# Kernel optimization log

Hardware: AMD Instinct MI355X
Metric: run time of the kernel (lower is better)

Reference implementation:

```python
import jax, jax.numpy as jnp
import numpy as np

T, D_ENC, H, D_EMB, VOCAB = 4000, 1024, 1024, 512, 8192
V = VOCAB + 1  # + blank
P = 800
TEMPERATURE = 1.0


def setup_inputs() -> dict:
    key = jax.random.key(0)
    ks = jax.random.split(key, 8)
    s = lambda d: 1.0 / np.sqrt(d)
    return {
        'enc_out': jax.random.normal(ks[0], (T, D_ENC), jnp.float32),
        'embedding': jax.random.normal(ks[1], (V, D_EMB), jnp.float32) * s(D_EMB),
        'W_ih': jax.random.normal(ks[2], (4 * H, D_EMB), jnp.float32) * s(D_EMB),
        'W_hh': jax.random.normal(ks[3], (4 * H, H), jnp.float32) * s(H),
        'b_lstm': jnp.zeros((4 * H,), jnp.float32),
        'W_pred': jax.random.normal(ks[4], (D_ENC, H), jnp.float32) * s(H),
        'b_pred': jnp.zeros((D_ENC,), jnp.float32),
        'W_join': jax.random.normal(ks[5], (V, D_ENC), jnp.float32) * s(D_ENC),
        'b_join': jnp.zeros((V,), jnp.float32),
        'phonemes': jax.random.randint(ks[6], (P,), 0, VOCAB, jnp.int32),
    }


def reference(enc_out, embedding, W_ih, W_hh, b_lstm, W_pred, b_pred, W_join, b_join, phonemes):
    blank_idx = embedding.shape[0] - 1
    n_phon = phonemes.shape[0]

    def predict_step(tok, h, c):
        # one-token RNNT predictor: embed -> LSTM cell -> projection to joiner dim
        x = embedding[tok]
        gates = x @ W_ih.T + h @ W_hh.T + b_lstm  # [4H]
        i, f, g, o = jnp.split(gates, 4)
        i, f, o = jax.nn.sigmoid(i), jax.nn.sigmoid(f), jax.nn.sigmoid(o)
        c2 = f * c + i * jnp.tanh(g)
        h2 = o * jnp.tanh(c2)
        pred = h2 @ W_pred.T + b_pred  # [D_ENC]
        return pred, h2, c2

    def step(carry, enc_t):
        tok, h, c, tp = carry
        pred, h2, c2 = predict_step(tok, h, c)
        logits = (jax.nn.relu(enc_t + pred) @ W_join.T + b_join) / TEMPERATURE
        logp = jax.nn.log_softmax(logits)  # [V]
        pick = jnp.argmax(logp)
        phon_done = tp >= n_phon
        is_blank = (pick == blank_idx) | phon_done
        next_phon = phonemes[jnp.minimum(tp, n_phon - 1)]
        prediction = jnp.where(is_blank, blank_idx, next_phon)
        # blank: keep hypothesis token/state; non-blank: advance to phoneme + new state
        tok2 = jnp.where(is_blank, tok, next_phon)
        h3 = jnp.where(is_blank, h, h2)
        c3 = jnp.where(is_blank, c, c2)
        tp2 = tp + jnp.where(is_blank, 0, 1)
        return (tok2, h3, c3, tp2), (logp, prediction, ~phon_done)

    # initial predictor pass with blank token from zero state (mirrors the warm-up predict call)
    h0 = jnp.zeros((W_hh.shape[1],), enc_out.dtype)
    c0 = jnp.zeros_like(h0)
    _, h_init, c_init = predict_step(jnp.int32(blank_idx), h0, c0)
    carry0 = (jnp.int32(blank_idx), h_init, c_init, jnp.int32(0))
    _, (alignment, predictions, valid) = jax.lax.scan(step, carry0, enc_out)
    return alignment, predictions, valid
```

## Files before the change

kernel.cpp:

```cpp
#include <hip/hip_runtime.h>
#include <math.h>

#define TT     4000
#define DENC   1024
#define HD     1024
#define DEMB   512
#define VD     8193
#define NPH    800
#define BLANK  8192
#define NWG    256
#define NTHR   512
#define CHUNK  256
#define CHUNK_M 800
#define NSTEP  (NPH + 2)
#define NVT    65
#define NP     129

typedef __bf16 bf16x4 __attribute__((ext_vector_type(4)));
typedef __bf16 bf16x8 __attribute__((ext_vector_type(8)));
typedef float  f32x16 __attribute__((ext_vector_type(16)));

#define FLAGS_BYTES  4096
#define MEMSET_BYTES 20480
#define WSF_HX     1024
#define WSF_HHIST  5120
#define WSF_PREDS  826368
#define WSF_PMAX_M 1646592
#define WSF_PSUM_M 2162592
#define WSF_PARG_M 2678592
#define WSF_LSE_M  3194592
#define WSF_AMAX_M 3198592
#define WSF_W16    3199616
#define WSF_XBF    7459456
#define WSF_END_M  9163392
#define NEED_MFMA  ((size_t)WSF_END_M * 4)
#define F_PMAX 1646592
#define F_PSUM 1906592
#define F_PARG 2166592
#define F_LSE  2426592

#define S_XH   0
#define S_GS   3072
#define S_C4   3088
#define S_TOK  3264
#define S_RED  4066
#define S_AMAX 4082
#define SMEM_FLOATS_F32 4352
#define SMEM_BYTES_F32 (SMEM_FLOATS_F32 * 4)
#define SMEM_BYTES_MFMA (65536 + 128)

struct Ctx {
  const float *enc, *emb, *Wih, *Whh, *bl, *Wpred, *bp, *Wjoin, *bj;
  const int* phon;
  unsigned long long* hx;
  float *hhist, *preds, *pmax, *psum, *lse;
  int* parg;
  int* amaxws;
  __bf16 *w16, *xbf;
  unsigned* flags;
  float *out_align, *out_pred, *out_valid;
};

__device__ __forceinline__ float dot4(float4 a, float4 b, float acc) {
  acc = fmaf(a.x, b.x, acc); acc = fmaf(a.y, b.y, acc);
  acc = fmaf(a.z, b.z, acc); acc = fmaf(a.w, b.w, acc);
  return acc;
}
__device__ __forceinline__ float sigmf(float x) { return 1.f / (1.f + expf(-x)); }

__device__ __forceinline__ void combine3(float& m, float& s, int& am,
                                         float om, float os, int oa) {
  float mm = fmaxf(m, om);
  s = s * __expf(m - mm) + os * __expf(om - mm);
  if (om > m || (om == m && oa < am)) am = oa;
  m = mm;
}

__device__ __forceinline__ void gload16(const void* g, void* l) {
  __builtin_amdgcn_global_load_lds(
      (const __attribute__((address_space(1))) unsigned int*)g,
      (__attribute__((address_space(3))) unsigned int*)l, 16, 0, 0);
}

__device__ __forceinline__ void light_barrier(unsigned* flags, unsigned& ep) {
  unsigned* arrive  = flags;
  unsigned* release = flags + 256;
  __builtin_amdgcn_s_waitcnt(0);
  __syncthreads();
  if (blockIdx.x == 0) {
    int tid = threadIdx.x;
    if (tid > 0 && tid < NWG) {
      while (__hip_atomic_load(&arrive[tid], __ATOMIC_RELAXED, __HIP_MEMORY_SCOPE_AGENT) != ep) {}
    }
    __syncthreads();
    if (tid == 0)
      __hip_atomic_store(release, ep, __ATOMIC_RELAXED, __HIP_MEMORY_SCOPE_AGENT);
  } else {
    if (threadIdx.x == 0) {
      __hip_atomic_store(&arrive[blockIdx.x], ep, __ATOMIC_RELAXED, __HIP_MEMORY_SCOPE_AGENT);
      while (__hip_atomic_load(release, __ATOMIC_RELAXED, __HIP_MEMORY_SCOPE_AGENT) != ep) {}
    }
    __syncthreads();
  }
  asm volatile("" ::: "memory");
  ep++;
}

__device__ __forceinline__ void heavy_barrier(unsigned* flags) {
  unsigned* bar = flags + 257;
  __syncthreads();
  if (threadIdx.x == 0) {
    __threadfence();
    unsigned g = __hip_atomic_load(&bar[1], __ATOMIC_RELAXED, __HIP_MEMORY_SCOPE_AGENT);
    unsigned v = __hip_atomic_fetch_add(&bar[0], 1u, __ATOMIC_RELAXED, __HIP_MEMORY_SCOPE_AGENT);
    if (v == (unsigned)(NWG - 1)) {
      __hip_atomic_store(&bar[0], 0u, __ATOMIC_RELAXED, __HIP_MEMORY_SCOPE_AGENT);
      __hip_atomic_store(&bar[1], g + 1u, __ATOMIC_RELEASE, __HIP_MEMORY_SCOPE_AGENT);
    } else {
      while (__hip_atomic_load(&bar[1], __ATOMIC_RELAXED, __HIP_MEMORY_SCOPE_AGENT) == g)
        __builtin_amdgcn_s_sleep(1);
    }
    __threadfence();
  }
  __syncthreads();
}

__device__ __forceinline__ float ld_coh(const float* p) {
  return __hip_atomic_load((const float*)p, __ATOMIC_RELAXED, __HIP_MEMORY_SCOPE_AGENT);
}

__device__ void chain_all(const Ctx& C, float* sm) {
  const int tid = threadIdx.x;
  const int w = tid >> 6, l = tid & 63;
  const int b = blockIdx.x;
  int* tok_sm = (int*)(sm + S_TOK);

  for (int s = tid; s < NSTEP; s += NTHR)
    tok_sm[s] = (s < 2) ? BLANK : C.phon[s - 2];

  float4 W0[6], W1[6];
  {
    int rr0 = 2 * w, rr1 = 2 * w + 1;
    int gr0 = ((rr0 >> 2) << 10) + 4 * b + (rr0 & 3);
    int gr1 = ((rr1 >> 2) << 10) + 4 * b + (rr1 & 3);
    const float4* ih0 = (const float4*)(C.Wih + (size_t)gr0 * DEMB);
    const float4* hh0 = (const float4*)(C.Whh + (size_t)gr0 * HD);
    const float4* ih1 = (const float4*)(C.Wih + (size_t)gr1 * DEMB);
    const float4* hh1 = (const float4*)(C.Whh + (size_t)gr1 * HD);
    W0[0] = ih0[l];       W0[1] = ih0[64 + l];
    W0[2] = hh0[l];       W0[3] = hh0[64 + l];
    W0[4] = hh0[128 + l]; W0[5] = hh0[192 + l];
    W1[0] = ih1[l];       W1[1] = ih1[64 + l];
    W1[2] = hh1[l];       W1[3] = hh1[64 + l];
    W1[4] = hh1[128 + l]; W1[5] = hh1[192 + l];
  }
  float bi = 0.f, bf = 0.f, bg = 0.f, bo = 0.f;
  if (tid < 4) {
    bi = C.bl[4 * b + tid];
    bf = C.bl[1024 + 4 * b + tid];
    bg = C.bl[2048 + 4 * b + tid];
    bo = C.bl[3072 + 4 * b + tid];
    sm[S_C4 + tid] = 0.f;
  }
  for (int i = tid; i < 1536; i += NTHR) sm[S_XH + i] = 0.f;
  if (tid < 512) sm[S_XH + tid] = C.emb[(size_t)BLANK * DEMB + tid];
  __syncthreads();

  unsigned long long* hx = C.hx;
  for (int s = 0; s < NSTEP; ++s) {
    int p = s & 1;
    const float4* xh4 = (const float4*)(sm + S_XH + p * 1536);
    float a0 = 0.f, a1 = 0.f;
    #pragma unroll
    for (int i = 0; i < 6; ++i) {
      float4 v = xh4[i * 64 + l];
      a0 = dot4(W0[i], v, a0);
      a1 = dot4(W1[i], v, a1);
    }
    #pragma unroll
    for (int m = 32; m; m >>= 1) {
      a0 += __shfl_xor(a0, m, 64);
      a1 += __shfl_xor(a1, m, 64);
    }
    if (l == 0) { sm[S_GS + 2 * w] = a0; sm[S_GS + 2 * w + 1] = a1; }
    if (s + 1 < NSTEP && tid < 512)
      sm[S_XH + (1 - p) * 1536 + tid] = C.emb[(size_t)tok_sm[s + 1] * DEMB + tid];
    __syncthreads();
    if (tid < 4) {
      int j = tid;
      float gi = sm[S_GS + j]      + bi;
      float gf = sm[S_GS + 4 + j]  + bf;
      float gg = sm[S_GS + 8 + j]  + bg;
      float go = sm[S_GS + 12 + j] + bo;
      float cc = sm[S_C4 + j];
      float c2 = sigmf(gf) * cc + sigmf(gi) * tanhf(gg);
      float h2 = sigmf(go) * tanhf(c2);
      sm[S_C4 + j] = c2;
      int cell = 4 * b + j;
      C.hhist[(size_t)s * HD + cell] = h2;
      unsigned long long pk = ((unsigned long long)(unsigned)(s + 1) << 32)
                            | (unsigned long long)__float_as_uint(h2);
      __hip_atomic_store(&hx[(1 - p) * 1024 + cell], pk,
                         __ATOMIC_RELAXED, __HIP_MEMORY_SCOPE_AGENT);
    }
    if (s + 1 < NSTEP) {
      unsigned tg = (unsigned)(s + 1);
      #pragma unroll
      for (int kq = 0; kq < 2; ++kq) {
        int k = tid + kq * 512;
        unsigned long long v;
        do {
          v = __hip_atomic_load(&hx[(1 - p) * 1024 + k],
                                __ATOMIC_RELAXED, __HIP_MEMORY_SCOPE_AGENT);
        } while ((unsigned)(v >> 32) != tg);
        sm[S_XH + (1 - p) * 1536 + 512 + k] = __uint_as_float((unsigned)v);
      }
    }
    __syncthreads();
  }
}

__device__ void preds_gemm(const Ctx& C, float* sm) {
  float* Wt = sm;
  float* Xt = sm + 2112;
  const int tid = threadIdx.x;
  const int tx = tid & 31, ty = tid >> 5;
  const int NJT = (NPH + 1 + 63) >> 6;
  int ntiles = 8 * NJT;
  for (int tile = blockIdx.x; tile < ntiles; tile += NWG) {
    int vt = tile & 7, jt = tile >> 3;
    int v0 = vt * 128, j0 = jt * 64;
    float acc[4][4];
    #pragma unroll
    for (int a = 0; a < 4; ++a)
      #pragma unroll
      for (int q = 0; q < 4; ++q) acc[a][q] = 0.f;
    for (int kk = 0; kk < 1024; kk += 16) {
      {
        int r = tid >> 2, seg = tid & 3;
        float4 wv = ((const float4*)(C.Wpred + (size_t)(v0 + r) * HD + kk))[seg];
        Wt[(seg * 4 + 0) * 132 + r] = wv.x;
        Wt[(seg * 4 + 1) * 132 + r] = wv.y;
        Wt[(seg * 4 + 2) * 132 + r] = wv.z;
        Wt[(seg * 4 + 3) * 132 + r] = wv.w;
      }
      if (tid < 256) {
        int r = tid >> 2, seg = tid & 3;
        int j = j0 + r;
        float4 xv = make_float4(0.f, 0.f, 0.f, 0.f);
        if (j <= NPH) xv = ((const float4*)(C.hhist + (size_t)(j + 1) * HD + kk))[seg];
        Xt[(seg * 4 + 0) * 68 + r] = xv.x;
        Xt[(seg * 4 + 1) * 68 + r] = xv.y;
        Xt[(seg * 4 + 2) * 68 + r] = xv.z;
        Xt[(seg * 4 + 3) * 68 + r] = xv.w;
      }
      __syncthreads();
      #pragma unroll
      for (int k = 0; k < 16; ++k) {
        float4 a = *(const float4*)(Wt + k * 132 + (tx << 2));
        float4 bq = *(const float4*)(Xt + k * 68 + (ty << 2));
        acc[0][0] = fmaf(a.x, bq.x, acc[0][0]); acc[1][0] = fmaf(a.y, bq.x, acc[1][0]);
        acc[2][0] = fmaf(a.z, bq.x, acc[2][0]); acc[3][0] = fmaf(a.w, bq.x, acc[3][0]);
        acc[0][1] = fmaf(a.x, bq.y, acc[0][1]); acc[1][1] = fmaf(a.y, bq.y, acc[1][1]);
        acc[2][1] = fmaf(a.z, bq.y, acc[2][1]); acc[3][1] = fmaf(a.w, bq.y, acc[3][1]);
        acc[0][2] = fmaf(a.x, bq.z, acc[0][2]); acc[1][2] = fmaf(a.y, bq.z, acc[1][2]);
        acc[2][2] = fmaf(a.z, bq.z, acc[2][2]); acc[3][2] = fmaf(a.w, bq.z, acc[3][2]);
        acc[0][3] = fmaf(a.x, bq.w, acc[0][3]); acc[1][3] = fmaf(a.y, bq.w, acc[1][3]);
        acc[2][3] = fmaf(a.z, bq.w, acc[2][3]); acc[3][3] = fmaf(a.w, bq.w, acc[3][3]);
      }
      __syncthreads();
    }
    int vb = v0 + (tx << 2), jb0 = j0 + (ty << 2);
    #pragma unroll
    for (int jj = 0; jj < 4; ++jj) {
      int j = jb0 + jj;
      if (j > NPH) continue;
      #pragma unroll
      for (int q = 0; q < 4; ++q)
        C.preds[(size_t)j * 1024 + vb + q] = acc[q][jj] + C.bp[vb + q];
    }
  }
}


__device__ void xbf_pass(const Ctx& C, int t0, int K, int pi0) {
  int g0 = blockIdx.x * NTHR + threadIdx.x;
  int total = K << 8;
  for (int q = g0; q < total; q += NWG * NTHR) {
    int j = q >> 8, seg = q & 255;
    int pi = (pi0 < 0) ? NPH : pi0 + j;
    float4 e = ((const float4*)(C.enc + (size_t)(t0 + j) * 1024))[seg];
    float4 p = ((const float4*)(C.preds + (size_t)pi * 1024))[seg];
    bf16x4 r;
    r[0] = (__bf16)fmaxf(e.x + p.x, 0.f);
    r[1] = (__bf16)fmaxf(e.y + p.y, 0.f);
    r[2] = (__bf16)fmaxf(e.z + p.z, 0.f);
    r[3] = (__bf16)fmaxf(e.w + p.w, 0.f);
    *(bf16x4*)(C.xbf + (size_t)j * 1024 + (seg << 2)) = r;
  }
}

__device__ void joiner_mfma(const Ctx& C, char* smc, int t0, int K) {
  const int tid = threadIdx.x;
  const int wid = tid >> 6, lane = tid & 63;
  const int wj = wid & 3, wv = wid >> 2;
  const int l31 = lane & 31, lhi = lane >> 5;
  const int jt_n = (K + 127) >> 7;
  const int ntiles = jt_n * NVT;
  const __bf16* W16 = C.w16;
  const __bf16* Xbf = C.xbf;

  for (int tile = blockIdx.x; tile < ntiles; tile += NWG) {
    const int vt = tile % NVT, jt = tile / NVT;
    const int v0 = vt << 7, j0 = jt << 7;
    f32x16 acc0, acc1;
    #pragma unroll
    for (int i = 0; i < 16; ++i) { acc0[i] = 0.f; acc1[i] = 0.f; }

    auto stage = [&](int db, int kb) {
      char* wb = smc + db * 32768;
      char* xb = wb + 16384;
      #pragma unroll
      for (int p = 0; p < 2; ++p) {
        int sbase = p * 512 + wid * 64;
        int s = sbase + lane;
        int ks = s >> 7, r = s & 127;
        gload16(W16 + (size_t)(v0 + r) * 1024 + kb + ks * 8, wb + sbase * 16);
        gload16(Xbf + (size_t)(j0 + r) * 1024 + kb + ks * 8, xb + sbase * 16);
      }
    };

    stage(0, 0);
    __syncthreads();
    int db = 0;
    for (int kb16 = 0; kb16 < 16; ++kb16) {
      if (kb16 < 15) stage(db ^ 1, (kb16 + 1) << 6);
      const char* wb = smc + db * 32768;
      const char* xb = wb + 16384;
      #pragma unroll
      for (int k16 = 0; k16 < 4; ++k16) {
        int ks = k16 * 2 + lhi;
        bf16x8 a  = *(const bf16x8*)(xb + ((ks << 7) + (wj << 5) + l31) * 16);
        bf16x8 b0 = *(const bf16x8*)(wb + ((ks << 7) + (wv << 6) + l31) * 16);
        bf16x8 b1 = *(const bf16x8*)(wb + ((ks << 7) + (wv << 6) + 32 + l31) * 16);
        acc0 = __builtin_amdgcn_mfma_f32_32x32x16_bf16(a, b0, acc0, 0, 0, 0);
        acc1 = __builtin_amdgcn_mfma_f32_32x32x16_bf16(a, b1, acc1, 0, 0, 0);
      }
      __syncthreads();
      db ^= 1;
    }

    const int v_0 = v0 + (wv << 6) + l31;
    const int v_1 = v_0 + 32;
    const float bj0 = (v_0 < VD) ? C.bj[v_0] : 0.f;
    const float bj1 = (v_1 < VD) ? C.bj[v_1] : 0.f;
    const int jbase = j0 + (wj << 5) + 4 * lhi;
    const bool npok = (v0 + (wv << 6)) < VD;
    const int np = (v0 >> 6) + wv;
    #pragma unroll
    for (int reg = 0; reg < 16; ++reg) {
      int j = jbase + (reg & 3) + 8 * (reg >> 2);
      bool jok = j < K;
      float lg0 = acc0[reg] + bj0;
      float lg1 = acc1[reg] + bj1;
      if (jok) {
        size_t ro = (size_t)(t0 + j) * VD;
        if (v_0 < VD) C.out_align[ro + v_0] = lg0;
        if (v_1 < VD) C.out_align[ro + v_1] = lg1;
      }
      float l0 = (v_0 < VD) ? lg0 : -1e30f;
      float l1 = (v_1 < VD) ? lg1 : -1e30f;
      float m = fmaxf(l0, l1);
      float ss = 0.f;
      if (v_0 < VD) ss += __expf(l0 - m);
      if (v_1 < VD) ss += __expf(l1 - m);
      int am = (l1 > l0) ? v_1 : v_0;
      #pragma unroll
      for (int msk = 1; msk <= 16; msk <<= 1) {
        float om = __shfl_xor(m, msk, 64);
        float os = __shfl_xor(ss, msk, 64);
        int oa = __shfl_xor(am, msk, 64);
        float mm = fmaxf(m, om);
        ss = ss * __expf(m - mm) + os * __expf(om - mm);
        if (om > m || (om == m && oa < am)) am = oa;
        m = mm;
      }
      if (l31 == 0 && jok && npok) {
        size_t pb = (size_t)(t0 + j) * NP + np;
        __hip_atomic_store(&C.pmax[pb], m, __ATOMIC_RELAXED, __HIP_MEMORY_SCOPE_AGENT);
        __hip_atomic_store(&C.psum[pb], ss, __ATOMIC_RELAXED, __HIP_MEMORY_SCOPE_AGENT);
        __hip_atomic_store(&C.parg[pb], am, __ATOMIC_RELAXED, __HIP_MEMORY_SCOPE_AGENT);
      }
    }
  }
}

__device__ __forceinline__ void merge_row129(const Ctx& C, int row, int lane,
                                             float& m, float& s, int& am) {
  size_t b = (size_t)row * NP;
  m = ld_coh(C.pmax + b + lane);
  s = ld_coh(C.psum + b + lane);
  am = __hip_atomic_load(&C.parg[b + lane], __ATOMIC_RELAXED, __HIP_MEMORY_SCOPE_AGENT);
  {
    int i2 = lane + 64;
    float om = ld_coh(C.pmax + b + i2);
    float os = ld_coh(C.psum + b + i2);
    int oa = __hip_atomic_load(&C.parg[b + i2], __ATOMIC_RELAXED, __HIP_MEMORY_SCOPE_AGENT);
    combine3(m, s, am, om, os, oa);
  }
  if (lane == 0) {
    float om = ld_coh(C.pmax + b + 128);
    float os = ld_coh(C.psum + b + 128);
    int oa = __hip_atomic_load(&C.parg[b + 128], __ATOMIC_RELAXED, __HIP_MEMORY_SCOPE_AGENT);
    combine3(m, s, am, om, os, oa);
  }
  #pragma unroll
  for (int msk = 32; msk; msk >>= 1) {
    float om = __shfl_xor(m, msk, 64);
    float os = __shfl_xor(s, msk, 64);
    int oa = __shfl_xor(am, msk, 64);
    combine3(m, s, am, om, os, oa);
  }
}

__global__ __launch_bounds__(NTHR) void decode_kernel_mfma(
    const float* enc, const float* emb, const float* Wih, const float* Whh,
    const float* bl, const float* Wpred, const float* bp, const float* Wjoin,
    const float* bj, const int* phon, float* out, float* wsf) {
  extern __shared__ float sm[];
  char* smc = (char*)sm;
  Ctx C;
  C.enc = enc; C.emb = emb; C.Wih = Wih; C.Whh = Whh; C.bl = bl;
  C.Wpred = Wpred; C.bp = bp; C.Wjoin = Wjoin; C.bj = bj; C.phon = phon;
  C.flags = (unsigned*)wsf;
  C.hx = (unsigned long long*)(wsf + WSF_HX);
  C.hhist = wsf + WSF_HHIST;
  C.preds = wsf + WSF_PREDS;
  C.pmax = wsf + WSF_PMAX_M;
  C.psum = wsf + WSF_PSUM_M;
  C.parg = (int*)(wsf + WSF_PARG_M);
  C.lse = wsf + WSF_LSE_M;
  C.amaxws = (int*)(wsf + WSF_AMAX_M);
  C.w16 = (__bf16*)(wsf + WSF_W16);
  C.xbf = (__bf16*)(wsf + WSF_XBF);
  C.out_align = out;
  C.out_pred  = out + (size_t)TT * VD;
  C.out_valid = out + (size_t)TT * VD + TT;

  const int tid = threadIdx.x;
  const int wid = tid >> 6, lane = tid & 63;
  unsigned ep = 1;

  {
    int g0 = blockIdx.x * NTHR + tid;
    for (int q = g0; q < VD * 256; q += NWG * NTHR) {
      int v = q >> 8, seg = q & 255;
      float4 w4 = ((const float4*)(C.Wjoin + (size_t)v * 1024))[seg];
      bf16x4 r;
      r[0] = (__bf16)w4.x; r[1] = (__bf16)w4.y; r[2] = (__bf16)w4.z; r[3] = (__bf16)w4.w;
      *(bf16x4*)(C.w16 + (size_t)v * 1024 + (seg << 2)) = r;
    }
  }

  chain_all(C, sm);
  heavy_barrier(C.flags);
  preds_gemm(C, sm);
  heavy_barrier(C.flags);

  int t = 0, tp = 0;
  while (t < TT && tp < NPH) {
    int K = CHUNK_M;
    if (TT - t < K) K = TT - t;
    if (NPH - tp < K) K = NPH - tp;
    heavy_barrier(C.flags);
    xbf_pass(C, t, K, tp);
    heavy_barrier(C.flags);
    joiner_mfma(C, smc, t, K);
    light_barrier(C.flags, ep);

    for (int j = blockIdx.x * 8 + wid; j < K; j += NWG * 8) {
      float m, s; int am;
      merge_row129(C, t + j, lane, m, s, am);
      if (lane == 0) {
        __hip_atomic_store(&C.amaxws[j], am, __ATOMIC_RELAXED, __HIP_MEMORY_SCOPE_AGENT);
        C.lse[t + j] = m + logf(s);
      }
    }
    light_barrier(C.flags, ep);

    int cand = K;
    for (int idx = tid; idx < K; idx += NTHR) {
      int a = __hip_atomic_load(&C.amaxws[idx], __ATOMIC_RELAXED, __HIP_MEMORY_SCOPE_AGENT);
      if (a == BLANK && idx < cand) cand = idx;
    }
    #pragma unroll
    for (int msk = 32; msk; msk >>= 1) cand = min(cand, __shfl_xor(cand, msk, 64));
    int* red = (int*)(smc + 65536);
    if (lane == 0) red[wid] = cand;
    __syncthreads();
    if (tid == 0) {
      int mn = red[0];
      for (int w2 = 1; w2 < 8; ++w2) mn = min(mn, red[w2]);
      red[8] = mn;
    }
    __syncthreads();
    int jb = red[8];
    __syncthreads();
    int nacc = (jb < K) ? jb + 1 : K;
    int nadv = (jb < K) ? jb : K;
    if (blockIdx.x == 0) {
      for (int j = tid; j < nacc; j += NTHR) {
        C.out_pred[t + j] = (j == jb) ? (float)BLANK : (float)C.phon[tp + j];
        C.out_valid[t + j] = 1.f;
      }
    }
    t += nacc; tp += nadv;
  }

  if (t < TT) {
    int Kt = TT - t;
    heavy_barrier(C.flags);
    xbf_pass(C, t, Kt, -1);
    heavy_barrier(C.flags);
    joiner_mfma(C, smc, t, Kt);
    light_barrier(C.flags, ep);
    for (int j = blockIdx.x * 8 + wid; j < Kt; j += NWG * 8) {
      float m, s; int am;
      merge_row129(C, t + j, lane, m, s, am);
      if (lane == 0) C.lse[t + j] = m + logf(s);
    }
    const int gtid = blockIdx.x * NTHR + tid;
    for (int i = gtid; i < Kt; i += NWG * NTHR) {
      C.out_pred[t + i] = (float)BLANK;
      C.out_valid[t + i] = 0.f;
    }
  }

  heavy_barrier(C.flags);

  for (int row = blockIdx.x; row < TT; row += NWG) {
    float l = C.lse[row];
    float* p = C.out_align + (size_t)row * VD;
    for (int i = tid; i < VD; i += NTHR) p[i] -= l;
  }
}


__device__ void joiner_gemm_f32(const Ctx& C, float* sm, int t0, int K, int pi0) {
  float* Wt = sm;
  float* Xt = sm + 2112;
  const int tid = threadIdx.x;
  const int tx = tid & 31, ty = tid >> 5;
  int jt_n = (K + 63) >> 6;
  int ntiles = jt_n * NVT;
  for (int tile = blockIdx.x; tile < ntiles; tile += NWG) {
    int vt = tile % NVT, jt = tile / NVT;
    int v0 = vt * 128, j0 = jt * 64;
    float acc[4][4];
    #pragma unroll
    for (int a = 0; a < 4; ++a)
      #pragma unroll
      for (int q = 0; q < 4; ++q) acc[a][q] = 0.f;

    for (int kk = 0; kk < 1024; kk += 16) {
      {
        int r = tid >> 2, seg = tid & 3;
        int v = v0 + r;
        float4 wv = make_float4(0.f, 0.f, 0.f, 0.f);
        if (v < VD) wv = ((const float4*)(C.Wjoin + (size_t)v * 1024 + kk))[seg];
        Wt[(seg * 4 + 0) * 132 + r] = wv.x;
        Wt[(seg * 4 + 1) * 132 + r] = wv.y;
        Wt[(seg * 4 + 2) * 132 + r] = wv.z;
        Wt[(seg * 4 + 3) * 132 + r] = wv.w;
      }
      if (tid < 256) {
        int r = tid >> 2, seg = tid & 3;
        int j = j0 + r;
        float4 xv = make_float4(0.f, 0.f, 0.f, 0.f);
        if (j < K) {
          int pi = (pi0 < 0) ? NPH : (pi0 + j);
          float4 e = ((const float4*)(C.enc + (size_t)(t0 + j) * DENC + kk))[seg];
          float4 pr = ((const float4*)(C.preds + (size_t)pi * 1024 + kk))[seg];
          xv.x = fmaxf(e.x + pr.x, 0.f);
          xv.y = fmaxf(e.y + pr.y, 0.f);
          xv.z = fmaxf(e.z + pr.z, 0.f);
          xv.w = fmaxf(e.w + pr.w, 0.f);
        }
        Xt[(seg * 4 + 0) * 68 + r] = xv.x;
        Xt[(seg * 4 + 1) * 68 + r] = xv.y;
        Xt[(seg * 4 + 2) * 68 + r] = xv.z;
        Xt[(seg * 4 + 3) * 68 + r] = xv.w;
      }
      __syncthreads();
      #pragma unroll
      for (int k = 0; k < 16; ++k) {
        float4 a = *(const float4*)(Wt + k * 132 + (tx << 2));
        float4 bq = *(const float4*)(Xt + k * 68 + (ty << 2));
        acc[0][0] = fmaf(a.x, bq.x, acc[0][0]); acc[1][0] = fmaf(a.y, bq.x, acc[1][0]);
        acc[2][0] = fmaf(a.z, bq.x, acc[2][0]); acc[3][0] = fmaf(a.w, bq.x, acc[3][0]);
        acc[0][1] = fmaf(a.x, bq.y, acc[0][1]); acc[1][1] = fmaf(a.y, bq.y, acc[1][1]);
        acc[2][1] = fmaf(a.z, bq.y, acc[2][1]); acc[3][1] = fmaf(a.w, bq.y, acc[3][1]);
        acc[0][2] = fmaf(a.x, bq.z, acc[0][2]); acc[1][2] = fmaf(a.y, bq.z, acc[1][2]);
        acc[2][2] = fmaf(a.z, bq.z, acc[2][2]); acc[3][2] = fmaf(a.w, bq.z, acc[3][2]);
        acc[0][3] = fmaf(a.x, bq.w, acc[0][3]); acc[1][3] = fmaf(a.y, bq.w, acc[1][3]);
        acc[2][3] = fmaf(a.z, bq.w, acc[2][3]); acc[3][3] = fmaf(a.w, bq.w, acc[3][3]);
      }
      __syncthreads();
    }
    int vb = v0 + (tx << 2);
    int jb0 = j0 + (ty << 2);
    float bjv[4];
    #pragma unroll
    for (int q = 0; q < 4; ++q) bjv[q] = (vb + q < VD) ? C.bj[vb + q] : 0.f;
    #pragma unroll
    for (int jj = 0; jj < 4; ++jj) {
      int j = jb0 + jj;
      if (j >= K) continue;
      size_t ro = (size_t)(t0 + j) * VD;
      float lg[4];
      float m = -1e30f; int am = vb;
      #pragma unroll
      for (int q = 0; q < 4; ++q) {
        int v = vb + q;
        if (v < VD) {
          lg[q] = acc[q][jj] + bjv[q];
          C.out_align[ro + v] = lg[q];
          if (lg[q] > m) { m = lg[q]; am = v; }
        } else lg[q] = -1e30f;
      }
      float ss = 0.f;
      #pragma unroll
      for (int q = 0; q < 4; ++q)
        if (vb + q < VD) ss += __expf(lg[q] - m);
      #pragma unroll
      for (int msk = 16; msk; msk >>= 1) {
        float om = __shfl_xor(m, msk, 64);
        float os = __shfl_xor(ss, msk, 64);
        int oa = __shfl_xor(am, msk, 64);
        combine3(m, ss, am, om, os, oa);
      }
      if (tx == 0) {
        size_t pb = (size_t)(t0 + j) * NVT + vt;
        __hip_atomic_store(&C.pmax[pb], m, __ATOMIC_RELAXED, __HIP_MEMORY_SCOPE_AGENT);
        __hip_atomic_store(&C.psum[pb], ss, __ATOMIC_RELAXED, __HIP_MEMORY_SCOPE_AGENT);
        __hip_atomic_store(&C.parg[pb], am, __ATOMIC_RELAXED, __HIP_MEMORY_SCOPE_AGENT);
      }
    }
  }
}

__device__ __forceinline__ void merge_row65(const Ctx& C, int row, int lane,
                                            float& m, float& s, int& am) {
  size_t b = (size_t)row * NVT;
  m = ld_coh(C.pmax + b + lane);
  s = ld_coh(C.psum + b + lane);
  am = __hip_atomic_load(&C.parg[b + lane], __ATOMIC_RELAXED, __HIP_MEMORY_SCOPE_AGENT);
  if (lane == 0) {
    float om = ld_coh(C.pmax + b + 64);
    float os = ld_coh(C.psum + b + 64);
    int oa = __hip_atomic_load(&C.parg[b + 64], __ATOMIC_RELAXED, __HIP_MEMORY_SCOPE_AGENT);
    combine3(m, s, am, om, os, oa);
  }
  #pragma unroll
  for (int msk = 32; msk; msk >>= 1) {
    float om = __shfl_xor(m, msk, 64);
    float os = __shfl_xor(s, msk, 64);
    int oa = __shfl_xor(am, msk, 64);
    combine3(m, s, am, om, os, oa);
  }
}

__global__ __launch_bounds__(NTHR) void decode_kernel_f32(
    const float* enc, const float* emb, const float* Wih, const float* Whh,
    const float* bl, const float* Wpred, const float* bp, const float* Wjoin,
    const float* bj, const int* phon, float* out, float* wsf) {
  extern __shared__ float sm[];
  Ctx C;
  C.enc = enc; C.emb = emb; C.Wih = Wih; C.Whh = Whh; C.bl = bl;
  C.Wpred = Wpred; C.bp = bp; C.Wjoin = Wjoin; C.bj = bj; C.phon = phon;
  C.flags = (unsigned*)wsf;
  C.hx = (unsigned long long*)(wsf + WSF_HX);
  C.hhist = wsf + WSF_HHIST;
  C.preds = wsf + WSF_PREDS;
  C.pmax = wsf + F_PMAX;
  C.psum = wsf + F_PSUM;
  C.parg = (int*)(wsf + F_PARG);
  C.lse = wsf + F_LSE;
  C.amaxws = 0; C.w16 = 0; C.xbf = 0;
  C.out_align = out;
  C.out_pred  = out + (size_t)TT * VD;
  C.out_valid = out + (size_t)TT * VD + TT;

  const int tid = threadIdx.x;
  const int wid = tid >> 6, lane = tid & 63;
  unsigned ep = 1;

  chain_all(C, sm);
  heavy_barrier(C.flags);
  preds_gemm(C, sm);
  heavy_barrier(C.flags);

  int t = 0, tp = 0;
  while (t < TT && tp < NPH) {
    int K = CHUNK;
    if (TT - t < K) K = TT - t;
    if (NPH - tp < K) K = NPH - tp;
    joiner_gemm_f32(C, sm, t, K, tp);
    light_barrier(C.flags, ep);

    int* amax_l = (int*)(sm + S_AMAX);
    for (int j = wid; j < K; j += 8) {
      float m, s; int am;
      merge_row65(C, t + j, lane, m, s, am);
      if (lane == 0) {
        amax_l[j] = am;
        C.lse[t + j] = m + logf(s);
      }
    }
    __syncthreads();
    int cand = K;
    if (tid < K && amax_l[tid] == BLANK) cand = tid;
    #pragma unroll
    for (int msk = 32; msk; msk >>= 1) cand = min(cand, __shfl_xor(cand, msk, 64));
    int* red = (int*)(sm + S_RED);
    if (lane == 0) red[wid] = cand;
    __syncthreads();
    if (tid == 0) {
      int mn = red[0];
      for (int w2 = 1; w2 < 8; ++w2) mn = min(mn, red[w2]);
      red[8] = mn;
    }
    __syncthreads();
    int jb = red[8];
    __syncthreads();
    int nacc = (jb < K) ? jb + 1 : K;
    int nadv = (jb < K) ? jb : K;
    if (blockIdx.x == 0) {
      int* tok_sm = (int*)(sm + S_TOK);
      for (int j = tid; j < nacc; j += NTHR) {
        C.out_pred[t + j] = (j == jb) ? (float)BLANK : (float)tok_sm[tp + j + 2];
        C.out_valid[t + j] = 1.f;
      }
    }
    t += nacc; tp += nadv;
    if (jb < K) heavy_barrier(C.flags);
  }

  if (t < TT) {
    int Kt = TT - t;
    joiner_gemm_f32(C, sm, t, Kt, -1);
    light_barrier(C.flags, ep);
    for (int i = blockIdx.x * 8 + wid; i < Kt; i += NWG * 8) {
      float m, s; int am;
      merge_row65(C, t + i, lane, m, s, am);
      if (lane == 0) C.lse[t + i] = m + logf(s);
    }
    const int gtid = blockIdx.x * NTHR + tid;
    for (int i = gtid; i < Kt; i += NWG * NTHR) {
      C.out_pred[t + i] = (float)BLANK;
      C.out_valid[t + i] = 0.f;
    }
  }

  heavy_barrier(C.flags);

  for (int row = blockIdx.x; row < TT; row += NWG) {
    float l = C.lse[row];
    float* p = C.out_align + (size_t)row * VD;
    for (int i = tid; i < VD; i += NTHR) p[i] -= l;
  }
}

extern "C" void kernel_launch(void* const* d_in, const int* in_sizes, int n_in,
                              void* d_out, int out_size, void* d_ws, size_t ws_size,
                              hipStream_t stream) {
  const float* enc   = (const float*)d_in[0];
  const float* emb   = (const float*)d_in[1];
  const float* Wih   = (const float*)d_in[2];
  const float* Whh   = (const float*)d_in[3];
  const float* bl    = (const float*)d_in[4];
  const float* Wpred = (const float*)d_in[5];
  const float* bp    = (const float*)d_in[6];
  const float* Wjoin = (const float*)d_in[7];
  const float* bj    = (const float*)d_in[8];
  const int*   phon  = (const int*)d_in[9];
  float* out = (float*)d_out;
  float* wsf = (float*)d_ws;

  hipMemsetAsync(d_ws, 0, MEMSET_BYTES, stream);

  void* args[] = { &enc, &emb, &Wih, &Whh, &bl, &Wpred, &bp, &Wjoin, &bj, &phon, &out, &wsf };
  if (ws_size >= NEED_MFMA) {
    hipFuncSetAttribute((const void*)decode_kernel_mfma,
                        hipFuncAttributeMaxDynamicSharedMemorySize, SMEM_BYTES_MFMA);
    hipError_t e = hipLaunchCooperativeKernel((void*)decode_kernel_mfma, dim3(NWG), dim3(NTHR),
                                              args, SMEM_BYTES_MFMA, stream);
    if (e != hipSuccess) {
      decode_kernel_mfma<<<dim3(NWG), dim3(NTHR), SMEM_BYTES_MFMA, stream>>>(
          enc, emb, Wih, Whh, bl, Wpred, bp, Wjoin, bj, phon, out, wsf);
    }
  } else {
    hipFuncSetAttribute((const void*)decode_kernel_f32,
                        hipFuncAttributeMaxDynamicSharedMemorySize, SMEM_BYTES_F32);
    hipError_t e = hipLaunchCooperativeKernel((void*)decode_kernel_f32, dim3(NWG), dim3(NTHR),
                                              args, SMEM_BYTES_F32, stream);
    if (e != hipSuccess) {
      decode_kernel_f32<<<dim3(NWG), dim3(NTHR), SMEM_BYTES_F32, stream>>>(
          enc, emb, Wih, Whh, bl, Wpred, bp, Wjoin, bj, phon, out, wsf);
    }
  }
}
```

Before: 2.850 ms.

## Split monolithic cooperative decode into staged kernels with speculative joiner

Replaces the single cooperative MFMA decode kernel with a pipeline of separate kernels: Wjoin bf16 conversion, a batched input-gate GEMM over all phoneme embeddings, a recurrence-only LSTM chain kernel holding W_hh in registers, a predictor GEMM, a speculative joiner over precomputed rows, a cooperative decode kernel, a tail joiner and final log-softmax subtraction. It moves the embedding-to-gate work off the serial recurrence and uses fast exp-based sigmoid/tanh. The aim is to shorten the sequential critical path and avoid grid-wide barriers between phases. The cost is more kernel launches and possibly wasted speculative joiner work, plus slightly lower-precision activations.

```diff
diff --git a/kernel.cpp b/kernel.cpp
--- a/kernel.cpp
+++ b/kernel.cpp
@@ -10,35 +10,40 @@
 #define BLANK  8192
 #define NWG    256
 #define NTHR   512
-#define CHUNK  256
 #define CHUNK_M 800
 #define NSTEP  (NPH + 2)
+#define NSTEPP 802
 #define NVT    65
 #define NP     129
+#define CHUNK  256
 
 typedef __bf16 bf16x4 __attribute__((ext_vector_type(4)));
 typedef __bf16 bf16x8 __attribute__((ext_vector_type(8)));
 typedef float  f32x16 __attribute__((ext_vector_type(16)));
 
-#define FLAGS_BYTES  4096
 #define MEMSET_BYTES 20480
 #define WSF_HX     1024
 #define WSF_HHIST  5120
 #define WSF_PREDS  826368
-#define WSF_PMAX_M 1646592
-#define WSF_PSUM_M 2162592
-#define WSF_PARG_M 2678592
-#define WSF_LSE_M  3194592
-#define WSF_AMAX_M 3198592
-#define WSF_W16    3199616
-#define WSF_XBF    7459456
-#define WSF_END_M  9163392
-#define NEED_MFMA  ((size_t)WSF_END_M * 4)
+#define WSF_GXT    826368
+#define WSF_PMAX   1646592
+#define WSF_PSUM   2162592
+#define WSF_PARG   2678592
+#define WSF_LSE    3194592
+#define WSF_AMAX   3198592
+#define WSF_XBF    3199616
+#define WSF_W16    4903552
+#define WSF_END    9163392
+#define NEED_MFMA  ((size_t)WSF_END * 4)
+#define TST_IDX    512
 #define F_PMAX 1646592
 #define F_PSUM 1906592
 #define F_PARG 2166592
 #define F_LSE  2426592
 
+#define GEMM_SMEM  12800
+#define CHAIN_SMEM ((16 * NSTEPP + 2048 + 64) * 4)
+#define JOIN_SMEM  (65536 + 128)
 #define S_XH   0
 #define S_GS   3072
 #define S_C4   3088
@@ -47,19 +52,7 @@
 #define S_AMAX 4082
 #define SMEM_FLOATS_F32 4352
 #define SMEM_BYTES_F32 (SMEM_FLOATS_F32 * 4)
-#define SMEM_BYTES_MFMA (65536 + 128)
-
-struct Ctx {
-  const float *enc, *emb, *Wih, *Whh, *bl, *Wpred, *bp, *Wjoin, *bj;
-  const int* phon;
-  unsigned long long* hx;
-  float *hhist, *preds, *pmax, *psum, *lse;
-  int* parg;
-  int* amaxws;
-  __bf16 *w16, *xbf;
-  unsigned* flags;
-  float *out_align, *out_pred, *out_valid;
-};
+
 
 __device__ __forceinline__ float dot4(float4 a, float4 b, float acc) {
   acc = fmaf(a.x, b.x, acc); acc = fmaf(a.y, b.y, acc);
@@ -67,6 +60,11 @@
   return acc;
 }
 __device__ __forceinline__ float sigmf(float x) { return 1.f / (1.f + expf(-x)); }
+__device__ __forceinline__ float sigm_fast(float x) { return 1.f / (1.f + __expf(-x)); }
+__device__ __forceinline__ float tanh_fast(float x) {
+  float e = __expf(2.f * x);
+  return 1.f - 2.f / (e + 1.f);
+}
 
 __device__ __forceinline__ void combine3(float& m, float& s, int& am,
                                          float om, float os, int oa) {
@@ -80,6 +78,10 @@
   __builtin_amdgcn_global_load_lds(
       (const __attribute__((address_space(1))) unsigned int*)g,
       (__attribute__((address_space(3))) unsigned int*)l, 16, 0, 0);
+}
+
+__device__ __forceinline__ float ld_coh(const float* p) {
+  return __hip_atomic_load((const float*)p, __ATOMIC_RELAXED, __HIP_MEMORY_SCOPE_AGENT);
 }
 
 __device__ __forceinline__ void light_barrier(unsigned* flags, unsigned& ep) {
@@ -125,19 +127,521 @@
   __syncthreads();
 }
 
-__device__ __forceinline__ float ld_coh(const float* p) {
-  return __hip_atomic_load((const float*)p, __ATOMIC_RELAXED, __HIP_MEMORY_SCOPE_AGENT);
-}
-
-__device__ void chain_all(const Ctx& C, float* sm) {
+__device__ void xbf_fill(const float* enc, const float* preds, __bf16* dst,
+                         int t0, int K, int pi0, int g0, int gs) {
+  int total = K << 8;
+  for (int q = g0; q < total; q += gs) {
+    int j = q >> 8, seg = q & 255;
+    int pi = (pi0 < 0) ? NPH : pi0 + j;
+    float4 e = ((const float4*)(enc + (size_t)(t0 + j) * 1024))[seg];
+    float4 p = ((const float4*)(preds + (size_t)pi * 1024))[seg];
+    bf16x4 r;
+    r[0] = (__bf16)fmaxf(e.x + p.x, 0.f);
+    r[1] = (__bf16)fmaxf(e.y + p.y, 0.f);
+    r[2] = (__bf16)fmaxf(e.z + p.z, 0.f);
+    r[3] = (__bf16)fmaxf(e.w + p.w, 0.f);
+    *(bf16x4*)(dst + (size_t)j * 1024 + (seg << 2)) = r;
+  }
+}
+
+__device__ void joiner_tiles(const __bf16* W16, const __bf16* xrows, const float* bj,
+                             float* out_align, float* pmax, float* psum, int* parg,
+                             char* smc, int t0, int K, int tile0, int tstride) {
+  const int tid = threadIdx.x;
+  const int wid = tid >> 6, lane = tid & 63;
+  const int wj = wid & 3, wv = wid >> 2;
+  const int l31 = lane & 31, lhi = lane >> 5;
+  const int jt_n = (K + 127) >> 7;
+  const int ntiles = jt_n * NVT;
+
+  for (int tile = tile0; tile < ntiles; tile += tstride) {
+    const int vt = tile % NVT, jt = tile / NVT;
+    const int v0 = vt << 7, j0 = jt << 7;
+    f32x16 acc0, acc1;
+    #pragma unroll
+    for (int i = 0; i < 16; ++i) { acc0[i] = 0.f; acc1[i] = 0.f; }
+
+    auto stage = [&](int db, int kb) {
+      char* wb = smc + db * 32768;
+      char* xb = wb + 16384;
+      #pragma unroll
+      for (int p = 0; p < 2; ++p) {
+        int sbase = p * 512 + wid * 64;
+        int s = sbase + lane;
+        int ks = s >> 7, r = s & 127;
+        gload16(W16 + (size_t)(v0 + r) * 1024 + kb + ks * 8, wb + sbase * 16);
+        gload16(xrows + (size_t)(j0 + r) * 1024 + kb + ks * 8, xb + sbase * 16);
+      }
+    };
+
+    stage(0, 0);
+    __syncthreads();
+    int db = 0;
+    for (int kb16 = 0; kb16 < 16; ++kb16) {
+      if (kb16 < 15) stage(db ^ 1, (kb16 + 1) << 6);
+      const char* wb = smc + db * 32768;
+      const char* xb = wb + 16384;
+      #pragma unroll
+      for (int k16 = 0; k16 < 4; ++k16) {
+        int ks = k16 * 2 + lhi;
+        bf16x8 a  = *(const bf16x8*)(xb + ((ks << 7) + (wj << 5) + l31) * 16);
+        bf16x8 b0 = *(const bf16x8*)(wb + ((ks << 7) + (wv << 6) + l31) * 16);
+        bf16x8 b1 = *(const bf16x8*)(wb + ((ks << 7) + (wv << 6) + 32 + l31) * 16);
+        acc0 = __builtin_amdgcn_mfma_f32_32x32x16_bf16(a, b0, acc0, 0, 0, 0);
+        acc1 = __builtin_amdgcn_mfma_f32_32x32x16_bf16(a, b1, acc1, 0, 0, 0);
+      }
+      __syncthreads();
+      db ^= 1;
+    }
+
+    const int v_0 = v0 + (wv << 6) + l31;
+    const int v_1 = v_0 + 32;
+    const float bj0 = (v_0 < VD) ? bj[v_0] : 0.f;
+    const float bj1 = (v_1 < VD) ? bj[v_1] : 0.f;
+    const int jbase = j0 + (wj << 5) + 4 * lhi;
+    const bool npok = (v0 + (wv << 6)) < VD;
+    const int np = (v0 >> 6) + wv;
+    #pragma unroll
+    for (int reg = 0; reg < 16; ++reg) {
+      int j = jbase + (reg & 3) + 8 * (reg >> 2);
+      bool jok = j < K;
+      float lg0 = acc0[reg] + bj0;
+      float lg1 = acc1[reg] + bj1;
+      if (jok) {
+        size_t ro = (size_t)(t0 + j) * VD;
+        if (v_0 < VD) out_align[ro + v_0] = lg0;
+        if (v_1 < VD) out_align[ro + v_1] = lg1;
+      }
+      float l0 = (v_0 < VD) ? lg0 : -1e30f;
+      float l1 = (v_1 < VD) ? lg1 : -1e30f;
+      float m = fmaxf(l0, l1);
+      float ss = 0.f;
+      if (v_0 < VD) ss += __expf(l0 - m);
+      if (v_1 < VD) ss += __expf(l1 - m);
+      int am = (l1 > l0) ? v_1 : v_0;
+      #pragma unroll
+      for (int msk = 1; msk <= 16; msk <<= 1) {
+        float om = __shfl_xor(m, msk, 64);
+        float os = __shfl_xor(ss, msk, 64);
+        int oa = __shfl_xor(am, msk, 64);
+        float mm = fmaxf(m, om);
+        ss = ss * __expf(m - mm) + os * __expf(om - mm);
+        if (om > m || (om == m && oa < am)) am = oa;
+        m = mm;
+      }
+      if (l31 == 0 && jok && npok) {
+        size_t pb = (size_t)(t0 + j) * NP + np;
+        __hip_atomic_store(&pmax[pb], m, __ATOMIC_RELAXED, __HIP_MEMORY_SCOPE_AGENT);
+        __hip_atomic_store(&psum[pb], ss, __ATOMIC_RELAXED, __HIP_MEMORY_SCOPE_AGENT);
+        __hip_atomic_store(&parg[pb], am, __ATOMIC_RELAXED, __HIP_MEMORY_SCOPE_AGENT);
+      }
+    }
+  }
+}
+
+__device__ __forceinline__ void merge_row129(const float* pmax, const float* psum,
+                                             const int* parg, int row, int lane,
+                                             float& m, float& s, int& am) {
+  size_t b = (size_t)row * NP;
+  m = ld_coh(pmax + b + lane);
+  s = ld_coh(psum + b + lane);
+  am = __hip_atomic_load(&parg[b + lane], __ATOMIC_RELAXED, __HIP_MEMORY_SCOPE_AGENT);
+  {
+    int i2 = lane + 64;
+    float om = ld_coh(pmax + b + i2);
+    float os = ld_coh(psum + b + i2);
+    int oa = __hip_atomic_load(&parg[b + i2], __ATOMIC_RELAXED, __HIP_MEMORY_SCOPE_AGENT);
+    combine3(m, s, am, om, os, oa);
+  }
+  if (lane == 0) {
+    float om = ld_coh(pmax + b + 128);
+    float os = ld_coh(psum + b + 128);
+    int oa = __hip_atomic_load(&parg[b + 128], __ATOMIC_RELAXED, __HIP_MEMORY_SCOPE_AGENT);
+    combine3(m, s, am, om, os, oa);
+  }
+  #pragma unroll
+  for (int msk = 32; msk; msk >>= 1) {
+    float om = __shfl_xor(m, msk, 64);
+    float os = __shfl_xor(s, msk, 64);
+    int oa = __shfl_xor(am, msk, 64);
+    combine3(m, s, am, om, os, oa);
+  }
+}
+
+__global__ __launch_bounds__(512) void wconv_kernel(const float* __restrict__ Wjoin,
+                                                    float* wsf) {
+  __bf16* w16 = (__bf16*)(wsf + WSF_W16);
+  int g0 = blockIdx.x * 512 + threadIdx.x;
+  int gs = gridDim.x * 512;
+  for (int q = g0; q < VD * 256; q += gs) {
+    int v = q >> 8, seg = q & 255;
+    float4 w4 = ((const float4*)(Wjoin + (size_t)v * 1024))[seg];
+    bf16x4 r;
+    r[0] = (__bf16)w4.x; r[1] = (__bf16)w4.y; r[2] = (__bf16)w4.z; r[3] = (__bf16)w4.w;
+    *(bf16x4*)(w16 + (size_t)v * 1024 + (seg << 2)) = r;
+  }
+}
+
+__global__ __launch_bounds__(512) void gx_kernel(
+    const float* __restrict__ Wih, const float* __restrict__ emb,
+    const float* __restrict__ bl, const int* __restrict__ phon, float* wsf) {
+  extern __shared__ float sm[];
+  float* Wt = sm;
+  float* Xt = sm + 2112;
+  float* gxT = wsf + WSF_GXT;
+  const int tid = threadIdx.x;
+  const int tx = tid & 31, ty = tid >> 5;
+  int ntiles = 32 * 13;
+  for (int tile = blockIdx.x; tile < ntiles; tile += gridDim.x) {
+    int vt = tile & 31, jt = tile >> 5;
+    int v0 = vt * 128, j0 = jt * 64;
+    float acc[4][4];
+    #pragma unroll
+    for (int a = 0; a < 4; ++a)
+      #pragma unroll
+      for (int q = 0; q < 4; ++q) acc[a][q] = 0.f;
+    for (int kk = 0; kk < DEMB; kk += 16) {
+      {
+        int r = tid >> 2, seg = tid & 3;
+        float4 wv = ((const float4*)(Wih + (size_t)(v0 + r) * DEMB + kk))[seg];
+        Wt[(seg * 4 + 0) * 132 + r] = wv.x;
+        Wt[(seg * 4 + 1) * 132 + r] = wv.y;
+        Wt[(seg * 4 + 2) * 132 + r] = wv.z;
+        Wt[(seg * 4 + 3) * 132 + r] = wv.w;
+      }
+      if (tid < 256) {
+        int r = tid >> 2, seg = tid & 3;
+        int j = j0 + r;
+        float4 xv = make_float4(0.f, 0.f, 0.f, 0.f);
+        if (j < NSTEP) {
+          int tok = (j < 2) ? BLANK : phon[j - 2];
+          xv = ((const float4*)(emb + (size_t)tok * DEMB + kk))[seg];
+        }
+        Xt[(seg * 4 + 0) * 68 + r] = xv.x;
+        Xt[(seg * 4 + 1) * 68 + r] = xv.y;
+        Xt[(seg * 4 + 2) * 68 + r] = xv.z;
+        Xt[(seg * 4 + 3) * 68 + r] = xv.w;
+      }
+      __syncthreads();
+      #pragma unroll
+      for (int k = 0; k < 16; ++k) {
+        float4 a = *(const float4*)(Wt + k * 132 + (tx << 2));
+        float4 bq = *(const float4*)(Xt + k * 68 + (ty << 2));
+        acc[0][0] = fmaf(a.x, bq.x, acc[0][0]); acc[1][0] = fmaf(a.y, bq.x, acc[1][0]);
+        acc[2][0] = fmaf(a.z, bq.x, acc[2][0]); acc[3][0] = fmaf(a.w, bq.x, acc[3][0]);
+        acc[0][1] = fmaf(a.x, bq.y, acc[0][1]); acc[1][1] = fmaf(a.y, bq.y, acc[1][1]);
+        acc[2][1] = fmaf(a.z, bq.y, acc[2][1]); acc[3][1] = fmaf(a.w, bq.y, acc[3][1]);
+        acc[0][2] = fmaf(a.x, bq.z, acc[0][2]); acc[1][2] = fmaf(a.y, bq.z, acc[1][2]);
+        acc[2][2] = fmaf(a.z, bq.z, acc[2][2]); acc[3][2] = fmaf(a.w, bq.z, acc[3][2]);
+        acc[0][3] = fmaf(a.x, bq.w, acc[0][3]); acc[1][3] = fmaf(a.y, bq.w, acc[1][3]);
+        acc[2][3] = fmaf(a.z, bq.w, acc[2][3]); acc[3][3] = fmaf(a.w, bq.w, acc[3][3]);
+      }
+      __syncthreads();
+    }
+    int vb = v0 + (tx << 2), jb0 = j0 + (ty << 2);
+    #pragma unroll
+    for (int jj = 0; jj < 4; ++jj) {
+      int j = jb0 + jj;
+      if (j >= NSTEP) continue;
+      #pragma unroll
+      for (int q = 0; q < 4; ++q)
+        gxT[(size_t)(vb + q) * NSTEPP + j] = acc[q][jj] + bl[vb + q];
+    }
+  }
+}
+
+__global__ __launch_bounds__(NTHR) void chain_kernel(const float* __restrict__ Whh,
+                                                     float* wsf) {
+  extern __shared__ float sm[];
+  float* gxl = sm;
+  float* hb  = sm + 16 * NSTEPP;
+  float* GS  = hb + 2048;
+  const int tid = threadIdx.x;
+  const int w = tid >> 6, l = tid & 63;
+  const int b = blockIdx.x;
+  const float* gxT = wsf + WSF_GXT;
+  float* hhist = wsf + WSF_HHIST;
+  unsigned long long* hx = (unsigned long long*)(wsf + WSF_HX);
+
+  float4 W0[4], W1[4];
+  {
+    int rr0 = 2 * w, rr1 = 2 * w + 1;
+    int gr0 = ((rr0 >> 2) << 10) + 4 * b + (rr0 & 3);
+    int gr1 = ((rr1 >> 2) << 10) + 4 * b + (rr1 & 3);
+    const float4* h0 = (const float4*)(Whh + (size_t)gr0 * HD);
+    const float4* h1 = (const float4*)(Whh + (size_t)gr1 * HD);
+    #pragma unroll
+    for (int i = 0; i < 4; ++i) { W0[i] = h0[l + 64 * i]; W1[i] = h1[l + 64 * i]; }
+  }
+  for (int rr = 0; rr < 16; ++rr) {
+    int gr = ((rr >> 2) << 10) + 4 * b + (rr & 3);
+    for (int s = tid; s < NSTEP; s += NTHR)
+      gxl[rr * NSTEPP + s] = gxT[(size_t)gr * NSTEPP + s];
+  }
+  for (int i = tid; i < 1024; i += NTHR) hb[i] = 0.f;
+  __syncthreads();
+
+  float c_reg = 0.f;
+  for (int s = 0; s < NSTEP; ++s) {
+    int p = s & 1;
+    const float4* h4 = (const float4*)(hb + p * 1024);
+    float a0 = 0.f, a1 = 0.f;
+    #pragma unroll
+    for (int i = 0; i < 4; ++i) {
+      float4 hv = h4[l + 64 * i];
+      a0 = dot4(W0[i], hv, a0);
+      a1 = dot4(W1[i], hv, a1);
+    }
+    #pragma unroll
+    for (int m = 32; m; m >>= 1) {
+      a0 += __shfl_xor(a0, m, 64);
+      a1 += __shfl_xor(a1, m, 64);
+    }
+    if (l == 0) { GS[2 * w] = a0; GS[2 * w + 1] = a1; }
+    __syncthreads();
+    if (tid < 4) {
+      int j = tid;
+      float gi = GS[j]      + gxl[j * NSTEPP + s];
+      float gf = GS[4 + j]  + gxl[(4 + j) * NSTEPP + s];
+      float gg = GS[8 + j]  + gxl[(8 + j) * NSTEPP + s];
+      float go = GS[12 + j] + gxl[(12 + j) * NSTEPP + s];
+      float c2 = sigm_fast(gf) * c_reg + sigm_fast(gi) * tanh_fast(gg);
+      float h2 = sigm_fast(go) * tanh_fast(c2);
+      c_reg = c2;
+      int cell = 4 * b + j;
+      hhist[(size_t)s * HD + cell] = h2;
+      unsigned long long pk = ((unsigned long long)(unsigned)(s + 1) << 32)
+                            | (unsigned long long)__float_as_uint(h2);
+      __hip_atomic_store(&hx[(p ^ 1) * 1024 + cell], pk,
+                         __ATOMIC_RELAXED, __HIP_MEMORY_SCOPE_AGENT);
+    }
+    if (s + 1 < NSTEP) {
+      unsigned tg = (unsigned)(s + 1);
+      const unsigned long long* src = hx + (p ^ 1) * 1024;
+      unsigned long long v0, v1;
+      do {
+        v0 = __hip_atomic_load(&src[2 * tid],     __ATOMIC_RELAXED, __HIP_MEMORY_SCOPE_AGENT);
+        v1 = __hip_atomic_load(&src[2 * tid + 1], __ATOMIC_RELAXED, __HIP_MEMORY_SCOPE_AGENT);
+      } while ((unsigned)(v0 >> 32) != tg || (unsigned)(v1 >> 32) != tg);
+      float* dst = hb + (p ^ 1) * 1024 + 2 * tid;
+      dst[0] = __uint_as_float((unsigned)v0);
+      dst[1] = __uint_as_float((unsigned)v1);
+    }
+    __syncthreads();
+  }
+}
+
+__global__ __launch_bounds__(512) void preds_kernel(
+    const float* __restrict__ Wpred, const float* __restrict__ bp, float* wsf) {
+  extern __shared__ float sm[];
+  float* Wt = sm;
+  float* Xt = sm + 2112;
+  const float* hhist = wsf + WSF_HHIST;
+  float* preds = wsf + WSF_PREDS;
+  const int tid = threadIdx.x;
+  const int tx = tid & 31, ty = tid >> 5;
+  int ntiles = 8 * 13;
+  for (int tile = blockIdx.x; tile < ntiles; tile += gridDim.x) {
+    int vt = tile & 7, jt = tile >> 3;
+    int v0 = vt * 128, j0 = jt * 64;
+    float acc[4][4];
+    #pragma unroll
+    for (int a = 0; a < 4; ++a)
+      #pragma unroll
+      for (int q = 0; q < 4; ++q) acc[a][q] = 0.f;
+    for (int kk = 0; kk < 1024; kk += 16) {
+      {
+        int r = tid >> 2, seg = tid & 3;
+        float4 wv = ((const float4*)(Wpred + (size_t)(v0 + r) * HD + kk))[seg];
+        Wt[(seg * 4 + 0) * 132 + r] = wv.x;
+        Wt[(seg * 4 + 1) * 132 + r] = wv.y;
+        Wt[(seg * 4 + 2) * 132 + r] = wv.z;
+        Wt[(seg * 4 + 3) * 132 + r] = wv.w;
+      }
+      if (tid < 256) {
+        int r = tid >> 2, seg = tid & 3;
+        int j = j0 + r;
+        float4 xv = make_float4(0.f, 0.f, 0.f, 0.f);
+        if (j <= NPH) xv = ((const float4*)(hhist + (size_t)(j + 1) * HD + kk))[seg];
+        Xt[(seg * 4 + 0) * 68 + r] = xv.x;
+        Xt[(seg * 4 + 1) * 68 + r] = xv.y;
+        Xt[(seg * 4 + 2) * 68 + r] = xv.z;
+        Xt[(seg * 4 + 3) * 68 + r] = xv.w;
+      }
+      __syncthreads();
+      #pragma unroll
+      for (int k = 0; k < 16; ++k) {
+        float4 a = *(const float4*)(Wt + k * 132 + (tx << 2));
+        float4 bq = *(const float4*)(Xt + k * 68 + (ty << 2));
+        acc[0][0] = fmaf(a.x, bq.x, acc[0][0]); acc[1][0] = fmaf(a.y, bq.x, acc[1][0]);
+        acc[2][0] = fmaf(a.z, bq.x, acc[2][0]); acc[3][0] = fmaf(a.w, bq.x, acc[3][0]);
+        acc[0][1] = fmaf(a.x, bq.y, acc[0][1]); acc[1][1] = fmaf(a.y, bq.y, acc[1][1]);
+        acc[2][1] = fmaf(a.z, bq.y, acc[2][1]); acc[3][1] = fmaf(a.w, bq.y, acc[3][1]);
+        acc[0][2] = fmaf(a.x, bq.z, acc[0][2]); acc[1][2] = fmaf(a.y, bq.z, acc[1][2]);
+        acc[2][2] = fmaf(a.z, bq.z, acc[2][2]); acc[3][2] = fmaf(a.w, bq.z, acc[3][2]);
+        acc[0][3] = fmaf(a.x, bq.w, acc[0][3]); acc[1][3] = fmaf(a.y, bq.w, acc[1][3]);
+        acc[2][3] = fmaf(a.z, bq.w, acc[2][3]); acc[3][3] = fmaf(a.w, bq.w, acc[3][3]);
+      }
+      __syncthreads();
+    }
+    int vb = v0 + (tx << 2), jb0 = j0 + (ty << 2);
+    #pragma unroll
+    for (int jj = 0; jj < 4; ++jj) {
+      int j = jb0 + jj;
+      if (j > NPH) continue;
+      #pragma unroll
+      for (int q = 0; q < 4; ++q)
+        preds[(size_t)j * 1024 + vb + q] = acc[q][jj] + bp[vb + q];
+    }
+  }
+}
+
+__global__ void xspec_kernel(const float* __restrict__ enc, float* wsf) {
+  xbf_fill(enc, wsf + WSF_PREDS, (__bf16*)(wsf + WSF_XBF), 0, CHUNK_M, 0,
+           blockIdx.x * blockDim.x + threadIdx.x, gridDim.x * blockDim.x);
+}
+
+__global__ __launch_bounds__(NTHR) void joinspec_kernel(const float* __restrict__ bj,
+                                                        float* out, float* wsf) {
+  extern __shared__ float sm[];
+  joiner_tiles((__bf16*)(wsf + WSF_W16), (__bf16*)(wsf + WSF_XBF), bj, out,
+               wsf + WSF_PMAX, wsf + WSF_PSUM, (int*)(wsf + WSF_PARG),
+               (char*)sm, 0, CHUNK_M, blockIdx.x, gridDim.x);
+}
+
+__global__ __launch_bounds__(NTHR) void decode_coop(
+    const float* enc, const float* bj, const int* phon, float* out, float* wsf) {
+  extern __shared__ float sm[];
+  char* smc = (char*)sm;
+  unsigned* flags = (unsigned*)wsf;
+  float* preds = wsf + WSF_PREDS;
+  float* pmax = wsf + WSF_PMAX;
+  float* psum = wsf + WSF_PSUM;
+  int* parg = (int*)(wsf + WSF_PARG);
+  float* lse = wsf + WSF_LSE;
+  int* amaxws = (int*)(wsf + WSF_AMAX);
+  __bf16* xbf = (__bf16*)(wsf + WSF_XBF);
+  __bf16* w16 = (__bf16*)(wsf + WSF_W16);
+  float* out_pred  = out + (size_t)TT * VD;
+  float* out_valid = out + (size_t)TT * VD + TT;
+
+  const int tid = threadIdx.x;
+  const int wid = tid >> 6, lane = tid & 63;
+  unsigned ep = 1;
+  int t = 0, tp = 0, iter = 0;
+
+  while (t < TT && tp < NPH) {
+    int K = CHUNK_M;
+    if (TT - t < K) K = TT - t;
+    if (NPH - tp < K) K = NPH - tp;
+    if (iter > 0) {
+      heavy_barrier(flags);
+      xbf_fill(enc, preds, xbf, t, K, tp, blockIdx.x * NTHR + tid, gridDim.x * NTHR);
+      heavy_barrier(flags);
+      joiner_tiles(w16, xbf, bj, out, pmax, psum, parg, smc, t, K,
+                   blockIdx.x, gridDim.x);
+    }
+    light_barrier(flags, ep);
+    for (int j = blockIdx.x * 8 + wid; j < K; j += gridDim.x * 8) {
+      float m, s; int am;
+      merge_row129(pmax, psum, parg, t + j, lane, m, s, am);
+      if (lane == 0) {
+        __hip_atomic_store(&amaxws[j], am, __ATOMIC_RELAXED, __HIP_MEMORY_SCOPE_AGENT);
+        lse[t + j] = m + logf(s);
+      }
+    }
+    light_barrier(flags, ep);
+    int cand = K;
+    for (int idx = tid; idx < K; idx += NTHR) {
+      int a = __hip_atomic_load(&amaxws[idx], __ATOMIC_RELAXED, __HIP_MEMORY_SCOPE_AGENT);
+      if (a == BLANK && idx < cand) cand = idx;
+    }
+    #pragma unroll
+    for (int msk = 32; msk; msk >>= 1) cand = min(cand, __shfl_xor(cand, msk, 64));
+    int* red = (int*)(smc + 65536);
+    if (lane == 0) red[wid] = cand;
+    __syncthreads();
+    if (tid == 0) {
+      int mn = red[0];
+      for (int w2 = 1; w2 < 8; ++w2) mn = min(mn, red[w2]);
+      red[8] = mn;
+    }
+    __syncthreads();
+    int jb = red[8];
+    __syncthreads();
+    int nacc = (jb < K) ? jb + 1 : K;
+    int nadv = (jb < K) ? jb : K;
+    if (blockIdx.x == 0) {
+      for (int j = tid; j < nacc; j += NTHR) {
+        out_pred[t + j] = (j == jb) ? (float)BLANK : (float)phon[tp + j];
+        out_valid[t + j] = 1.f;
+      }
+    }
+    t += nacc; tp += nadv; ++iter;
+  }
+
+  if (t < TT) {
+    xbf_fill(enc, preds, xbf + (size_t)(t - 800) * 1024, t, TT - t, -1,
+             blockIdx.x * NTHR + tid, gridDim.x * NTHR);
+  }
+  if (blockIdx.x == 0 && tid == 0) ((int*)wsf)[TST_IDX] = t;
+}
+
+__global__ __launch_bounds__(NTHR) void jointail_kernel(const float* __restrict__ bj,
+                                                        float* out, float* wsf) {
+  extern __shared__ float sm[];
+  int t = ((const int*)wsf)[TST_IDX];
+  if (t >= TT) return;
+  joiner_tiles((__bf16*)(wsf + WSF_W16),
+               (__bf16*)(wsf + WSF_XBF) + (size_t)(t - 800) * 1024, bj, out,
+               wsf + WSF_PMAX, wsf + WSF_PSUM, (int*)(wsf + WSF_PARG),
+               (char*)sm, t, TT - t, blockIdx.x, gridDim.x);
+}
+
+__global__ __launch_bounds__(NTHR) void mergetail_kernel(float* out, float* wsf) {
+  int t = ((const int*)wsf)[TST_IDX];
+  float* lse = wsf + WSF_LSE;
+  float* out_pred  = out + (size_t)TT * VD;
+  float* out_valid = out + (size_t)TT * VD + TT;
+  const int wid = threadIdx.x >> 6, lane = threadIdx.x & 63;
+  for (int row = t + blockIdx.x * 8 + wid; row < TT; row += gridDim.x * 8) {
+    float m, s; int am;
+    merge_row129(wsf + WSF_PMAX, wsf + WSF_PSUM, (const int*)(wsf + WSF_PARG),
+                 row, lane, m, s, am);
+    if (lane == 0) {
+      lse[row] = m + logf(s);
+      out_pred[row] = (float)BLANK;
+      out_valid[row] = 0.f;
+    }
+  }
+}
+
+__global__ __launch_bounds__(256) void sub_kernel(float* out, const float* wsf) {
+  const float* lse = wsf + WSF_LSE;
+  for (int row = blockIdx.x; row < TT; row += gridDim.x) {
+    float l = lse[row];
+    float* p = out + (size_t)row * VD;
+    for (int i = threadIdx.x; i < VD; i += 256) p[i] -= l;
+  }
+}
+
+struct Ctx {
+  const float *enc, *emb, *Wih, *Whh, *bl, *Wpred, *bp, *Wjoin, *bj;
+  const int* phon;
+  unsigned long long* hx;
+  float *hhist, *preds, *pmax, *psum, *lse;
+  int* parg;
+  unsigned* flags;
+  float *out_align, *out_pred, *out_valid;
+};
+
+__device__ void chain_all_legacy(const Ctx& C, float* sm) {
   const int tid = threadIdx.x;
   const int w = tid >> 6, l = tid & 63;
   const int b = blockIdx.x;
   int* tok_sm = (int*)(sm + S_TOK);
-
   for (int s = tid; s < NSTEP; s += NTHR)
     tok_sm[s] = (s < 2) ? BLANK : C.phon[s - 2];
-
   float4 W0[6], W1[6];
   {
     int rr0 = 2 * w, rr1 = 2 * w + 1;
@@ -165,7 +669,6 @@
   for (int i = tid; i < 1536; i += NTHR) sm[S_XH + i] = 0.f;
   if (tid < 512) sm[S_XH + tid] = C.emb[(size_t)BLANK * DEMB + tid];
   __syncthreads();
-
   unsigned long long* hx = C.hx;
   for (int s = 0; s < NSTEP; ++s) {
     int p = s & 1;
@@ -220,13 +723,12 @@
   }
 }
 
-__device__ void preds_gemm(const Ctx& C, float* sm) {
+__device__ void preds_gemm_legacy(const Ctx& C, float* sm) {
   float* Wt = sm;
   float* Xt = sm + 2112;
   const int tid = threadIdx.x;
   const int tx = tid & 31, ty = tid >> 5;
-  const int NJT = (NPH + 1 + 63) >> 6;
-  int ntiles = 8 * NJT;
+  int ntiles = 8 * 13;
   for (int tile = blockIdx.x; tile < ntiles; tile += NWG) {
     int vt = tile & 7, jt = tile >> 3;
     int v0 = vt * 128, j0 = jt * 64;
@@ -282,270 +784,6 @@
   }
 }
 
-
-__device__ void xbf_pass(const Ctx& C, int t0, int K, int pi0) {
-  int g0 = blockIdx.x * NTHR + threadIdx.x;
-  int total = K << 8;
-  for (int q = g0; q < total; q += NWG * NTHR) {
-    int j = q >> 8, seg = q & 255;
-    int pi = (pi0 < 0) ? NPH : pi0 + j;
-    float4 e = ((const float4*)(C.enc + (size_t)(t0 + j) * 1024))[seg];
-    float4 p = ((const float4*)(C.preds + (size_t)pi * 1024))[seg];
-    bf16x4 r;
-    r[0] = (__bf16)fmaxf(e.x + p.x, 0.f);
-    r[1] = (__bf16)fmaxf(e.y + p.y, 0.f);
-    r[2] = (__bf16)fmaxf(e.z + p.z, 0.f);
-    r[3] = (__bf16)fmaxf(e.w + p.w, 0.f);
-    *(bf16x4*)(C.xbf + (size_t)j * 1024 + (seg << 2)) = r;
-  }
-}
-
-__device__ void joiner_mfma(const Ctx& C, char* smc, int t0, int K) {
-  const int tid = threadIdx.x;
-  const int wid = tid >> 6, lane = tid & 63;
-  const int wj = wid & 3, wv = wid >> 2;
-  const int l31 = lane & 31, lhi = lane >> 5;
-  const int jt_n = (K + 127) >> 7;
-  const int ntiles = jt_n * NVT;
-  const __bf16* W16 = C.w16;
-  const __bf16* Xbf = C.xbf;
-
-  for (int tile = blockIdx.x; tile < ntiles; tile += NWG) {
-    const int vt = tile % NVT, jt = tile / NVT;
-    const int v0 = vt << 7, j0 = jt << 7;
-    f32x16 acc0, acc1;
-    #pragma unroll
-    for (int i = 0; i < 16; ++i) { acc0[i] = 0.f; acc1[i] = 0.f; }
-
-    auto stage = [&](int db, int kb) {
-      char* wb = smc + db * 32768;
-      char* xb = wb + 16384;
-      #pragma unroll
-      for (int p = 0; p < 2; ++p) {
-        int sbase = p * 512 + wid * 64;
-        int s = sbase + lane;
-        int ks = s >> 7, r = s & 127;
-        gload16(W16 + (size_t)(v0 + r) * 1024 + kb + ks * 8, wb + sbase * 16);
-        gload16(Xbf + (size_t)(j0 + r) * 1024 + kb + ks * 8, xb + sbase * 16);
-      }
-    };
-
-    stage(0, 0);
-    __syncthreads();
-    int db = 0;
-    for (int kb16 = 0; kb16 < 16; ++kb16) {
-      if (kb16 < 15) stage(db ^ 1, (kb16 + 1) << 6);
-      const char* wb = smc + db * 32768;
-      const char* xb = wb + 16384;
-      #pragma unroll
-      for (int k16 = 0; k16 < 4; ++k16) {
-        int ks = k16 * 2 + lhi;
-        bf16x8 a  = *(const bf16x8*)(xb + ((ks << 7) + (wj << 5) + l31) * 16);
-        bf16x8 b0 = *(const bf16x8*)(wb + ((ks << 7) + (wv << 6) + l31) * 16);
-        bf16x8 b1 = *(const bf16x8*)(wb + ((ks << 7) + (wv << 6) + 32 + l31) * 16);
-        acc0 = __builtin_amdgcn_mfma_f32_32x32x16_bf16(a, b0, acc0, 0, 0, 0);
-        acc1 = __builtin_amdgcn_mfma_f32_32x32x16_bf16(a, b1, acc1, 0, 0, 0);
-      }
-      __syncthreads();
-      db ^= 1;
-    }
-
-    const int v_0 = v0 + (wv << 6) + l31;
-    const int v_1 = v_0 + 32;
-    const float bj0 = (v_0 < VD) ? C.bj[v_0] : 0.f;
-    const float bj1 = (v_1 < VD) ? C.bj[v_1] : 0.f;
-    const int jbase = j0 + (wj << 5) + 4 * lhi;
-    const bool npok = (v0 + (wv << 6)) < VD;
-    const int np = (v0 >> 6) + wv;
-    #pragma unroll
-    for (int reg = 0; reg < 16; ++reg) {
-      int j = jbase + (reg & 3) + 8 * (reg >> 2);
-      bool jok = j < K;
-      float lg0 = acc0[reg] + bj0;
-      float lg1 = acc1[reg] + bj1;
-      if (jok) {
-        size_t ro = (size_t)(t0 + j) * VD;
-        if (v_0 < VD) C.out_align[ro + v_0] = lg0;
-        if (v_1 < VD) C.out_align[ro + v_1] = lg1;
-      }
-      float l0 = (v_0 < VD) ? lg0 : -1e30f;
-      float l1 = (v_1 < VD) ? lg1 : -1e30f;
-      float m = fmaxf(l0, l1);
-      float ss = 0.f;
-      if (v_0 < VD) ss += __expf(l0 - m);
-      if (v_1 < VD) ss += __expf(l1 - m);
-      int am = (l1 > l0) ? v_1 : v_0;
-      #pragma unroll
-      for (int msk = 1; msk <= 16; msk <<= 1) {
-        float om = __shfl_xor(m, msk, 64);
-        float os = __shfl_xor(ss, msk, 64);
-        int oa = __shfl_xor(am, msk, 64);
-        float mm = fmaxf(m, om);
-        ss = ss * __expf(m - mm) + os * __expf(om - mm);
-        if (om > m || (om == m && oa < am)) am = oa;
-        m = mm;
-      }
-      if (l31 == 0 && jok && npok) {
-        size_t pb = (size_t)(t0 + j) * NP + np;
-        __hip_atomic_store(&C.pmax[pb], m, __ATOMIC_RELAXED, __HIP_MEMORY_SCOPE_AGENT);
-        __hip_atomic_store(&C.psum[pb], ss, __ATOMIC_RELAXED, __HIP_MEMORY_SCOPE_AGENT);
-        __hip_atomic_store(&C.parg[pb], am, __ATOMIC_RELAXED, __HIP_MEMORY_SCOPE_AGENT);
-      }
-    }
-  }
-}
-
-__device__ __forceinline__ void merge_row129(const Ctx& C, int row, int lane,
-                                             float& m, float& s, int& am) {
-  size_t b = (size_t)row * NP;
-  m = ld_coh(C.pmax + b + lane);
-  s = ld_coh(C.psum + b + lane);
-  am = __hip_atomic_load(&C.parg[b + lane], __ATOMIC_RELAXED, __HIP_MEMORY_SCOPE_AGENT);
-  {
-    int i2 = lane + 64;
-    float om = ld_coh(C.pmax + b + i2);
-    float os = ld_coh(C.psum + b + i2);
-    int oa = __hip_atomic_load(&C.parg[b + i2], __ATOMIC_RELAXED, __HIP_MEMORY_SCOPE_AGENT);
-    combine3(m, s, am, om, os, oa);
-  }
-  if (lane == 0) {
-    float om = ld_coh(C.pmax + b + 128);
-    float os = ld_coh(C.psum + b + 128);
-    int oa = __hip_atomic_load(&C.parg[b + 128], __ATOMIC_RELAXED, __HIP_MEMORY_SCOPE_AGENT);
-    combine3(m, s, am, om, os, oa);
-  }
-  #pragma unroll
-  for (int msk = 32; msk; msk >>= 1) {
-    float om = __shfl_xor(m, msk, 64);
-    float os = __shfl_xor(s, msk, 64);
-    int oa = __shfl_xor(am, msk, 64);
-    combine3(m, s, am, om, os, oa);
-  }
-}
-
-__global__ __launch_bounds__(NTHR) void decode_kernel_mfma(
-    const float* enc, const float* emb, const float* Wih, const float* Whh,
-    const float* bl, const float* Wpred, const float* bp, const float* Wjoin,
-    const float* bj, const int* phon, float* out, float* wsf) {
-  extern __shared__ float sm[];
-  char* smc = (char*)sm;
-  Ctx C;
-  C.enc = enc; C.emb = emb; C.Wih = Wih; C.Whh = Whh; C.bl = bl;
-  C.Wpred = Wpred; C.bp = bp; C.Wjoin = Wjoin; C.bj = bj; C.phon = phon;
-  C.flags = (unsigned*)wsf;
-  C.hx = (unsigned long long*)(wsf + WSF_HX);
-  C.hhist = wsf + WSF_HHIST;
-  C.preds = wsf + WSF_PREDS;
-  C.pmax = wsf + WSF_PMAX_M;
-  C.psum = wsf + WSF_PSUM_M;
-  C.parg = (int*)(wsf + WSF_PARG_M);
-  C.lse = wsf + WSF_LSE_M;
-  C.amaxws = (int*)(wsf + WSF_AMAX_M);
-  C.w16 = (__bf16*)(wsf + WSF_W16);
-  C.xbf = (__bf16*)(wsf + WSF_XBF);
-  C.out_align = out;
-  C.out_pred  = out + (size_t)TT * VD;
-  C.out_valid = out + (size_t)TT * VD + TT;
-
-  const int tid = threadIdx.x;
-  const int wid = tid >> 6, lane = tid & 63;
-  unsigned ep = 1;
-
-  {
-    int g0 = blockIdx.x * NTHR + tid;
-    for (int q = g0; q < VD * 256; q += NWG * NTHR) {
-      int v = q >> 8, seg = q & 255;
-      float4 w4 = ((const float4*)(C.Wjoin + (size_t)v * 1024))[seg];
-      bf16x4 r;
-      r[0] = (__bf16)w4.x; r[1] = (__bf16)w4.y; r[2] = (__bf16)w4.z; r[3] = (__bf16)w4.w;
-      *(bf16x4*)(C.w16 + (size_t)v * 1024 + (seg << 2)) = r;
-    }
-  }
-
-  chain_all(C, sm);
-  heavy_barrier(C.flags);
-  preds_gemm(C, sm);
-  heavy_barrier(C.flags);
-
-  int t = 0, tp = 0;
-  while (t < TT && tp < NPH) {
-    int K = CHUNK_M;
-    if (TT - t < K) K = TT - t;
-    if (NPH - tp < K) K = NPH - tp;
-    heavy_barrier(C.flags);
-    xbf_pass(C, t, K, tp);
-    heavy_barrier(C.flags);
-    joiner_mfma(C, smc, t, K);
-    light_barrier(C.flags, ep);
-
-    for (int j = blockIdx.x * 8 + wid; j < K; j += NWG * 8) {
-      float m, s; int am;
-      merge_row129(C, t + j, lane, m, s, am);
-      if (lane == 0) {
-        __hip_atomic_store(&C.amaxws[j], am, __ATOMIC_RELAXED, __HIP_MEMORY_SCOPE_AGENT);
-        C.lse[t + j] = m + logf(s);
-      }
-    }
-    light_barrier(C.flags, ep);
-
-    int cand = K;
-    for (int idx = tid; idx < K; idx += NTHR) {
-      int a = __hip_atomic_load(&C.amaxws[idx], __ATOMIC_RELAXED, __HIP_MEMORY_SCOPE_AGENT);
-      if (a == BLANK && idx < cand) cand = idx;
-    }
-    #pragma unroll
-    for (int msk = 32; msk; msk >>= 1) cand = min(cand, __shfl_xor(cand, msk, 64));
-    int* red = (int*)(smc + 65536);
-    if (lane == 0) red[wid] = cand;
-    __syncthreads();
-    if (tid == 0) {
-      int mn = red[0];
-      for (int w2 = 1; w2 < 8; ++w2) mn = min(mn, red[w2]);
-      red[8] = mn;
-    }
-    __syncthreads();
-    int jb = red[8];
-    __syncthreads();
-    int nacc = (jb < K) ? jb + 1 : K;
-    int nadv = (jb < K) ? jb : K;
-    if (blockIdx.x == 0) {
-      for (int j = tid; j < nacc; j += NTHR) {
-        C.out_pred[t + j] = (j == jb) ? (float)BLANK : (float)C.phon[tp + j];
-        C.out_valid[t + j] = 1.f;
-      }
-    }
-    t += nacc; tp += nadv;
-  }
-
-  if (t < TT) {
-    int Kt = TT - t;
-    heavy_barrier(C.flags);
-    xbf_pass(C, t, Kt, -1);
-    heavy_barrier(C.flags);
-    joiner_mfma(C, smc, t, Kt);
-    light_barrier(C.flags, ep);
-    for (int j = blockIdx.x * 8 + wid; j < Kt; j += NWG * 8) {
-      float m, s; int am;
-      merge_row129(C, t + j, lane, m, s, am);
-      if (lane == 0) C.lse[t + j] = m + logf(s);
-    }
-    const int gtid = blockIdx.x * NTHR + tid;
-    for (int i = gtid; i < Kt; i += NWG * NTHR) {
-      C.out_pred[t + i] = (float)BLANK;
-      C.out_valid[t + i] = 0.f;
-    }
-  }
-
-  heavy_barrier(C.flags);
-
-  for (int row = blockIdx.x; row < TT; row += NWG) {
-    float l = C.lse[row];
-    float* p = C.out_align + (size_t)row * VD;
-    for (int i = tid; i < VD; i += NTHR) p[i] -= l;
-  }
-}
-
-
 __device__ void joiner_gemm_f32(const Ctx& C, float* sm, int t0, int K, int pi0) {
   float* Wt = sm;
   float* Xt = sm + 2112;
@@ -561,7 +799,6 @@
     for (int a = 0; a < 4; ++a)
       #pragma unroll
       for (int q = 0; q < 4; ++q) acc[a][q] = 0.f;
-
     for (int kk = 0; kk < 1024; kk += 16) {
       {
         int r = tid >> 2, seg = tid & 3;
@@ -686,7 +923,6 @@
   C.psum = wsf + F_PSUM;
   C.parg = (int*)(wsf + F_PARG);
   C.lse = wsf + F_LSE;
-  C.amaxws = 0; C.w16 = 0; C.xbf = 0;
   C.out_align = out;
   C.out_pred  = out + (size_t)TT * VD;
   C.out_valid = out + (size_t)TT * VD + TT;
@@ -695,9 +931,9 @@
   const int wid = tid >> 6, lane = tid & 63;
   unsigned ep = 1;
 
-  chain_all(C, sm);
+  chain_all_legacy(C, sm);
   heavy_barrier(C.flags);
-  preds_gemm(C, sm);
+  preds_gemm_legacy(C, sm);
   heavy_barrier(C.flags);
 
   int t = 0, tp = 0;
@@ -707,7 +943,6 @@
     if (NPH - tp < K) K = NPH - tp;
     joiner_gemm_f32(C, sm, t, K, tp);
     light_barrier(C.flags, ep);
-
     int* amax_l = (int*)(sm + S_AMAX);
     for (int j = wid; j < K; j += 8) {
       float m, s; int am;
@@ -745,7 +980,6 @@
     t += nacc; tp += nadv;
     if (jb < K) heavy_barrier(C.flags);
   }
-
   if (t < TT) {
     int Kt = TT - t;
     joiner_gemm_f32(C, sm, t, Kt, -1);
@@ -761,15 +995,14 @@
       C.out_valid[t + i] = 0.f;
     }
   }
-
   heavy_barrier(C.flags);
-
   for (int row = blockIdx.x; row < TT; row += NWG) {
     float l = C.lse[row];
     float* p = C.out_align + (size_t)row * VD;
     for (int i = tid; i < VD; i += NTHR) p[i] -= l;
   }
 }
+
 
 extern "C" void kernel_launch(void* const* d_in, const int* in_sizes, int n_in,
                               void* d_out, int out_size, void* d_ws, size_t ws_size,
@@ -789,19 +1022,45 @@
 
   hipMemsetAsync(d_ws, 0, MEMSET_BYTES, stream);
 
-  void* args[] = { &enc, &emb, &Wih, &Whh, &bl, &Wpred, &bp, &Wjoin, &bj, &phon, &out, &wsf };
   if (ws_size >= NEED_MFMA) {
-    hipFuncSetAttribute((const void*)decode_kernel_mfma,
-                        hipFuncAttributeMaxDynamicSharedMemorySize, SMEM_BYTES_MFMA);
-    hipError_t e = hipLaunchCooperativeKernel((void*)decode_kernel_mfma, dim3(NWG), dim3(NTHR),
-                                              args, SMEM_BYTES_MFMA, stream);
-    if (e != hipSuccess) {
-      decode_kernel_mfma<<<dim3(NWG), dim3(NTHR), SMEM_BYTES_MFMA, stream>>>(
-          enc, emb, Wih, Whh, bl, Wpred, bp, Wjoin, bj, phon, out, wsf);
-    }
+    hipFuncSetAttribute((const void*)chain_kernel,
+                        hipFuncAttributeMaxDynamicSharedMemorySize, CHAIN_SMEM);
+    hipFuncSetAttribute((const void*)joinspec_kernel,
+                        hipFuncAttributeMaxDynamicSharedMemorySize, JOIN_SMEM);
+    hipFuncSetAttribute((const void*)decode_coop,
+                        hipFuncAttributeMaxDynamicSharedMemorySize, JOIN_SMEM);
+    hipFuncSetAttribute((const void*)jointail_kernel,
+                        hipFuncAttributeMaxDynamicSharedMemorySize, JOIN_SMEM);
+
+    wconv_kernel<<<1024, 512, 0, stream>>>(Wjoin, wsf);
+    gx_kernel<<<416, 512, GEMM_SMEM, stream>>>(Wih, emb, bl, phon, wsf);
+    {
+      const float* WhhA = Whh; float* wsfA = wsf;
+      void* a2[] = { &WhhA, &wsfA };
+      hipError_t e = hipLaunchCooperativeKernel((void*)chain_kernel, dim3(256), dim3(NTHR),
+                                                a2, CHAIN_SMEM, stream);
+      if (e != hipSuccess)
+        chain_kernel<<<dim3(256), dim3(NTHR), CHAIN_SMEM, stream>>>(Whh, wsf);
+    }
+    preds_kernel<<<104, 512, GEMM_SMEM, stream>>>(Wpred, bp, wsf);
+    xspec_kernel<<<1024, 256, 0, stream>>>(enc, wsf);
+    joinspec_kernel<<<455, NTHR, JOIN_SMEM, stream>>>(bj, out, wsf);
+    {
+      const float* encA = enc; const float* bjA = bj; const int* phonA = phon;
+      float* outA = out; float* wsfA = wsf;
+      void* a3[] = { &encA, &bjA, &phonA, &outA, &wsfA };
+      hipError_t e = hipLaunchCooperativeKernel((void*)decode_coop, dim3(NWG), dim3(NTHR),
+                                                a3, JOIN_SMEM, stream);
+      if (e != hipSuccess)
+        decode_coop<<<dim3(NWG), dim3(NTHR), JOIN_SMEM, stream>>>(enc, bj, phon, out, wsf);
+    }
+    jointail_kernel<<<1664, NTHR, JOIN_SMEM, stream>>>(bj, out, wsf);
+    mergetail_kernel<<<256, NTHR, 0, stream>>>(out, wsf);
+    sub_kernel<<<2048, 256, 0, stream>>>(out, wsf);
   } else {
     hipFuncSetAttribute((const void*)decode_kernel_f32,
                         hipFuncAttributeMaxDynamicSharedMemorySize, SMEM_BYTES_F32);
+    void* args[] = { &enc, &emb, &Wih, &Whh, &bl, &Wpred, &bp, &Wjoin, &bj, &phon, &out, &wsf };
     hipError_t e = hipLaunchCooperativeKernel((void*)decode_kernel_f32, dim3(NWG), dim3(NTHR),
                                               args, SMEM_BYTES_F32, stream);
     if (e != hipSuccess) {
```

Result: faster. 2.705 ms (-5.1%).
